# Optimization experiments

Measured on AMD Instinct MI355X. Metric: run time of the kernel, lower is better.

The kernel has to match this reference:

```python
import jax, jax.numpy as jnp
import numpy as np

N = 4096   # num_nodes == nb_items
E = 3      # num_edge types
C = 2      # num_channels
D = 128    # basket_embed_dim
RU = 128   # rnn_units
B = 32     # batch size
L = 20     # max_seq_length
ALPHA = 0.5


def _gtconv(W, A):
    # softmax over edge types, then channel-weighted combine of adjacencies
    f = jax.nn.softmax(W, axis=1)              # [C, E]
    return jnp.einsum('ce,enm->cnm', f, A)     # [C, N, N]


def _normalize(H):
    # remove self loops, then column-degree (in-degree) inverse normalization
    eye = jnp.eye(H.shape[-1], dtype=H.dtype)
    Hn = H * (1.0 - eye)
    deg = Hn.sum(axis=1)                        # scatter_add over col -> [C, N]
    dinv = jnp.where(deg == 0, jnp.zeros_like(deg), 1.0 / deg)
    dinv = jax.lax.stop_gradient(dinv)          # original computes deg under no_grad
    return Hn * dinv[:, None, :]


def _lstm(x, h0, c0, W_ih, W_hh, b_ih, b_hh):
    # single-layer batch-first LSTM, torch gate order (i, f, g, o)
    def step(carry, xt):
        h, c = carry
        z = xt @ W_ih.T + b_ih + h @ W_hh.T + b_hh
        i, f, g, o = jnp.split(z, 4, axis=-1)
        c = jax.nn.sigmoid(f) * c + jax.nn.sigmoid(i) * jnp.tanh(g)
        h = jax.nn.sigmoid(o) * jnp.tanh(c)
        return (h, c), h
    _, ys = jax.lax.scan(step, (h0, c0), jnp.swapaxes(x, 0, 1))
    return jnp.swapaxes(ys, 0, 1)               # [B, L, RU]


def setup_inputs():
    key = jax.random.key(0)
    k = jax.random.split(key, 12)
    A = jax.random.uniform(k[0], (E, N, N), jnp.float32) * (2.0 / N)
    seqs = (jax.random.uniform(k[1], (B, L, N)) < 0.02).astype(jnp.float32)
    seq_len = jax.random.randint(k[2], (B,), 1, L + 1)
    h0 = jnp.zeros((B, RU), jnp.float32)
    c0 = jnp.zeros((B, RU), jnp.float32)
    W1a = 1.0 + 0.1 * jax.random.normal(k[3], (C, E), jnp.float32)
    W1b = 1.0 + 0.1 * jax.random.normal(k[4], (C, E), jnp.float32)
    W2 = 1.0 + 0.1 * jax.random.normal(k[5], (C, E), jnp.float32)
    I_B = jnp.ones((N,), jnp.float32) / N
    lin_w = jax.random.normal(k[6], (C, D, N), jnp.float32) / np.sqrt(N).astype(np.float32)
    lin_b = jnp.zeros((C, D), jnp.float32)
    proj_w = jax.random.normal(k[7], (D, C * D), jnp.float32) / np.sqrt(C * D).astype(np.float32)
    proj_b = jnp.zeros((D,), jnp.float32)
    W_ih = jax.random.normal(k[8], (4 * RU, D), jnp.float32) / np.sqrt(D).astype(np.float32)
    W_hh = jax.random.normal(k[9], (4 * RU, RU), jnp.float32) / np.sqrt(RU).astype(np.float32)
    b_ih = jnp.zeros((4 * RU,), jnp.float32)
    b_hh = jnp.zeros((4 * RU,), jnp.float32)
    h2item_w = jax.random.normal(k[10], (N, RU), jnp.float32) / np.sqrt(RU).astype(np.float32)
    return dict(A=A, seqs=seqs, seq_len=seq_len, h0=h0, c0=c0, W1a=W1a, W1b=W1b,
                W2=W2, I_B=I_B, lin_w=lin_w, lin_b=lin_b, proj_w=proj_w, proj_b=proj_b,
                W_ih=W_ih, W_hh=W_hh, b_ih=b_ih, b_hh=b_hh, h2item_w=h2item_w)


def reference(A, seqs, seq_len, h0, c0, W1a, W1b, W2, I_B, lin_w, lin_b,
              proj_w, proj_b, W_ih, W_hh, b_ih, b_hh, h2item_w):
    # layer 0 (first=True): H[c] = conv1(A)[c] @ conv2(A)[c]  (spspmm, dense form)
    H = jnp.einsum('cij,cjk->cik', _gtconv(W1a, A), _gtconv(W1b, A))
    # layer 1: H[c] = norm(H)[c] @ conv(A)[c]
    H = jnp.einsum('cij,cjk->cik', _normalize(H), _gtconv(W2, A))

    x = seqs.reshape(-1, N)                     # [B*L, nb_items]
    v = jax.nn.relu(I_B)                        # diag(I_B) after relu
    enc = []
    for i in range(C):
        xh = jax.nn.relu(x @ H[i])
        if i == 0:
            e = jax.nn.relu(x * v) + xh         # note: channel-0 formula differs
        else:
            e = jax.nn.relu(x * v + xh)
        enc.append(e @ lin_w[i].T + lin_b[i])
    enc = jnp.concatenate(enc, axis=1)          # [B*L, C*D]
    baskets = (enc @ proj_w.T + proj_b).reshape(B, L, D)

    lstm_out = _lstm(baskets, h0, c0, W_ih, W_hh, b_ih, b_hh)
    idx = jnp.arange(B) * L + (seq_len - 1)
    last = lstm_out.reshape(-1, RU)[idx]        # [B, RU]
    probs = jax.nn.sigmoid(last @ h2item_w.T)   # [B, nb_items]
    return (1.0 - ALPHA) * probs + ALPHA * (probs * v)
```

## Files before the change

kernel.cpp:

```cpp
#include <hip/hip_runtime.h>


typedef float  f4v  __attribute__((ext_vector_type(4)));
typedef short  s8v  __attribute__((ext_vector_type(8)));
typedef unsigned short u16;
typedef u16    us4  __attribute__((ext_vector_type(4)));

#define NN 4096
#define MM 640

__device__ __forceinline__ u16 f2bf(float f){
  unsigned int u = __float_as_uint(f);
  u += 0x7FFFu + ((u>>16)&1u);
  return (u16)(u>>16);
}
__device__ __forceinline__ float bf2f(u16 h){ return __uint_as_float(((unsigned int)h)<<16); }
__device__ __forceinline__ float sigm(float x){ return 1.f/(1.f+__expf(-x)); }

__device__ __forceinline__ void gload16(const void* g, void* l){
  __builtin_amdgcn_global_load_lds((const __attribute__((address_space(1))) unsigned int*)g,
                                   (__attribute__((address_space(3))) unsigned int*)l, 16, 0, 0);
}

__device__ __forceinline__ void softmax23(const float* __restrict__ W, float f[2][3]){
  #pragma unroll
  for (int c=0;c<2;c++){
    float a=W[c*3+0], b=W[c*3+1], d=W[c*3+2];
    float m=fmaxf(a,fmaxf(b,d));
    float ea=__expf(a-m), eb=__expf(b-m), ed=__expf(d-m);
    float s=1.f/(ea+eb+ed);
    f[c][0]=ea*s; f[c][1]=eb*s; f[c][2]=ed*s;
  }
}

template<int PH3>
__global__ __launch_bounds__(256)
void k_combine(const float* __restrict__ A, const float* __restrict__ Wa,
               const float* __restrict__ Wb, u16* __restrict__ C1,
               u16* __restrict__ Ct, float* __restrict__ r)
{
  __shared__ u16 t2[2][64][68];
  __shared__ float rs[2][64];
  const int tid = threadIdx.x;
  const int n0 = blockIdx.x*64, m0 = blockIdx.y*64;
  float fa[2][3], fb[2][3];
  softmax23(Wa, fa);
  if constexpr(!PH3) softmax23(Wb, fb);
  if constexpr(!PH3){ if (tid < 128) rs[tid>>6][tid&63] = 0.f; }
  __syncthreads();
  const int cl = (tid&15)*4, rw0 = tid>>4;
  float rp[2][4] = {};
  #pragma unroll
  for (int q=0;q<4;q++){
    const int m = q*16 + rw0;
    const float* ap = A + (size_t)(m0+m)*NN + n0 + cl;
    f4v a0 = *(const f4v*)ap;
    f4v a1 = *(const f4v*)(ap + (size_t)NN*NN);
    f4v a2 = *(const f4v*)(ap + 2*(size_t)NN*NN);
    #pragma unroll
    for (int c=0;c<2;c++){
      f4v vt;
      if constexpr(!PH3){
        f4v v1 = fa[c][0]*a0 + fa[c][1]*a1 + fa[c][2]*a2;
        vt     = fb[c][0]*a0 + fb[c][1]*a1 + fb[c][2]*a2;
        us4 o;
        #pragma unroll
        for (int k=0;k<4;k++){ o[k]=f2bf(v1[k]); rp[c][k]+=v1[k]; }
        *(us4*)(C1 + ((size_t)c*NN + m0+m)*NN + n0+cl) = o;
      } else {
        vt = fa[c][0]*a0 + fa[c][1]*a1 + fa[c][2]*a2;
      }
      #pragma unroll
      for (int k=0;k<4;k++) t2[c][cl+k][m] = f2bf(vt[k]);
    }
  }
  if constexpr(!PH3){
    #pragma unroll
    for (int c=0;c<2;c++)
      #pragma unroll
      for (int k=0;k<4;k++) atomicAdd(&rs[c][cl+k], rp[c][k]);
  }
  __syncthreads();
  if constexpr(!PH3){
    if (tid < 128) atomicAdd(&r[(size_t)(tid>>6)*NN + n0 + (tid&63)], rs[tid>>6][tid&63]);
  }
  #pragma unroll
  for (int q=0;q<4;q++){
    const int nl = q*16 + rw0;
    #pragma unroll
    for (int c=0;c<2;c++){
      us4 o = *(const us4*)&t2[c][nl][cl];
      *(us4*)(Ct + ((size_t)c*NN + n0+nl)*NN + m0+cl) = o;
    }
  }
}

__global__ __launch_bounds__(256)
void k_sparse_y(const float* __restrict__ seqs, const u16* __restrict__ C1,
                u16* __restrict__ y)
{
  __shared__ int idxl[512];
  __shared__ int cnt;
  const int tid = threadIdx.x, row = blockIdx.x;
  if (tid==0) cnt = 0;
  __syncthreads();
  const float* xr = seqs + (size_t)row*NN;
  #pragma unroll
  for (int it=0; it<4; ++it){
    f4v v = *(const f4v*)(xr + it*1024 + tid*4);
    #pragma unroll
    for (int k=0;k<4;k++) if (v[k] > 0.5f){ int p = atomicAdd(&cnt,1); if (p<512) idxl[p] = it*1024+tid*4+k; }
  }
  __syncthreads();
  const int nz = cnt < 512 ? cnt : 512;
  float acc0[16], acc1[16];
  #pragma unroll
  for (int k=0;k<16;k++){ acc0[k]=0.f; acc1[k]=0.f; }
  const int cb = tid*16;
  for (int p=0;p<nz;++p){
    const u16* r0 = C1 + (size_t)idxl[p]*NN + cb;
    const u16* r1 = r0 + (size_t)NN*NN;
    s8v a = *(const s8v*)r0, b = *(const s8v*)(r0+8);
    s8v c = *(const s8v*)r1, d = *(const s8v*)(r1+8);
    #pragma unroll
    for (int k=0;k<8;k++){
      acc0[k]   += bf2f((u16)a[k]);
      acc0[8+k] += bf2f((u16)b[k]);
      acc1[k]   += bf2f((u16)c[k]);
      acc1[8+k] += bf2f((u16)d[k]);
    }
  }
  s8v o0,o1,o2,o3;
  #pragma unroll
  for (int k=0;k<8;k++){
    o0[k]=(short)f2bf(acc0[k]);   o1[k]=(short)f2bf(acc0[8+k]);
    o2[k]=(short)f2bf(acc1[k]);   o3[k]=(short)f2bf(acc1[8+k]);
  }
  u16* y0 = y + (size_t)row*NN + cb;
  *(s8v*)y0 = o0; *(s8v*)(y0+8) = o1;
  u16* y1 = y0 + (size_t)MM*NN;
  *(s8v*)y1 = o2; *(s8v*)(y1+8) = o3;
}

__global__ __launch_bounds__(256)
void k_diagdeg(const u16* __restrict__ C1, const u16* __restrict__ C2t,
               const float* __restrict__ r, float* __restrict__ diag1,
               float* __restrict__ dinv)
{
  const int tid = threadIdx.x, lane = tid&63;
  const int gw = blockIdx.x*4 + (tid>>6);
  const int c = gw>>12, k = gw&4095;
  const u16* p1 = C1  + ((size_t)c*NN + k)*NN;
  const u16* p2 = C2t + ((size_t)c*NN + k)*NN;
  const float* pr = r + (size_t)c*NN;
  float dd = 0.f, dg = 0.f;
  for (int it=0; it<8; ++it){
    const int j = it*512 + lane*8;
    s8v v1 = *(const s8v*)(p1+j);
    s8v v2 = *(const s8v*)(p2+j);
    f4v r0 = *(const f4v*)(pr+j);
    f4v r1 = *(const f4v*)(pr+j+4);
    #pragma unroll
    for (int q=0;q<8;q++){
      float c2 = bf2f((u16)v2[q]);
      dd += bf2f((u16)v1[q]) * c2;
      dg += ((q<4)? r0[q] : r1[q-4]) * c2;
    }
  }
  #pragma unroll
  for (int m=1;m<64;m<<=1){ dd += __shfl_xor(dd, m); dg += __shfl_xor(dg, m); }
  if (lane==0){
    float deg = dg - dd;
    diag1[(size_t)c*NN+k] = dd;
    dinv[(size_t)c*NN+k]  = (deg==0.f) ? 0.f : 1.f/deg;
  }
}

template<int EPI>
__global__ __launch_bounds__(256)
void k_gemm(const u16* __restrict__ Xb, const u16* __restrict__ Bt,
            const float* __restrict__ seqs, const float* __restrict__ diag1,
            const float* __restrict__ dinv, const float* __restrict__ IB,
            u16* __restrict__ outp)
{
  __shared__ u16 As[128*32];
  __shared__ u16 Bs[128*32];
  const int tid = threadIdx.x, lane = tid&63, w = tid>>6;
  const int c = blockIdx.z, m0 = blockIdx.x*128, n0 = blockIdx.y*128;
  const u16* Ab = Xb + (size_t)c*MM*NN;
  const u16* Bb = Bt + (size_t)c*NN*NN;
  const int srow = lane>>2, skof = (lane&3)*8;
  const int fr = lane&15, fk = (lane>>4)*8;
  const int wm = (w>>1)*64, wn = (w&1)*64;
  f4v acc[4][4];
  #pragma unroll
  for (int i=0;i<4;i++)
    #pragma unroll
    for (int j=0;j<4;j++) acc[i][j] = (f4v){0.f,0.f,0.f,0.f};
  for (int k0=0;k0<NN;k0+=32){
    gload16(Ab + (size_t)(m0 +      w*16 + srow)*NN + k0 + skof, (void*)&As[(     w*16)*32]);
    gload16(Ab + (size_t)(m0 + 64 + w*16 + srow)*NN + k0 + skof, (void*)&As[(64 + w*16)*32]);
    gload16(Bb + (size_t)(n0 +      w*16 + srow)*NN + k0 + skof, (void*)&Bs[(     w*16)*32]);
    gload16(Bb + (size_t)(n0 + 64 + w*16 + srow)*NN + k0 + skof, (void*)&Bs[(64 + w*16)*32]);
    __syncthreads();
    s8v a[4], b[4];
    #pragma unroll
    for (int t=0;t<4;t++) a[t] = *(const s8v*)&As[(wm + t*16 + fr)*32 + fk];
    #pragma unroll
    for (int t=0;t<4;t++) b[t] = *(const s8v*)&Bs[(wn + t*16 + fr)*32 + fk];
    #pragma unroll
    for (int i=0;i<4;i++)
      #pragma unroll
      for (int j=0;j<4;j++)
        acc[i][j] = __builtin_amdgcn_mfma_f32_16x16x32_bf16(a[i], b[j], acc[i][j], 0, 0, 0);
    __syncthreads();
  }
  #pragma unroll
  for (int i=0;i<4;i++){
    #pragma unroll
    for (int j=0;j<4;j++){
      const int col = n0 + wn + j*16 + fr;
      #pragma unroll
      for (int rr=0;rr<4;rr++){
        const int row = m0 + wm + i*16 + (lane>>4)*4 + rr;
        const float z = acc[i][j][rr];
        const float x = seqs[(size_t)row*NN + col];
        float val;
        if constexpr(EPI==0){
          val = (z - x*diag1[(size_t)c*NN+col]) * dinv[(size_t)c*NN+col];
        } else {
          float xh = fmaxf(z, 0.f);
          float vv = fmaxf(IB[col], 0.f);
          val = (c==0) ? (fmaxf(x*vv,0.f) + xh) : fmaxf(x*vv + xh, 0.f);
        }
        outp[((size_t)c*MM + row)*NN + col] = f2bf(val);
      }
    }
  }
}

__global__ __launch_bounds__(256)
void k_cvt(const float* __restrict__ linw, const float* __restrict__ whh,
           u16* __restrict__ linwb, u16* __restrict__ whhb)
{
  const int g = blockIdx.x*256 + threadIdx.x;
  const int i = g*4;
  const int NL = 2*128*NN;
  f4v v; u16* dst;
  if (i < NL){ v = *(const f4v*)(linw + i); dst = linwb + i; }
  else       { v = *(const f4v*)(whh + (i-NL)); dst = whhb + (i-NL); }
  us4 o;
  #pragma unroll
  for (int k=0;k<4;k++) o[k]=f2bf(v[k]);
  *(us4*)dst = o;
}

__global__ __launch_bounds__(256)
void k_lin(const u16* __restrict__ e, const u16* __restrict__ linwb,
           float* __restrict__ encr)
{
  __shared__ u16 As[64*32];
  __shared__ u16 Bs[64*32];
  const int tid=threadIdx.x, lane=tid&63, w=tid>>6;
  const int m0 = blockIdx.x*64, d0 = blockIdx.y*64;
  const int c = blockIdx.z>>2, ks = blockIdx.z&3;
  const u16* Ab = e + (size_t)c*MM*NN;
  const u16* Bb = linwb + (size_t)c*128*NN;
  const int srow=lane>>2, skof=(lane&3)*8, fr=lane&15, fk=(lane>>4)*8;
  const int wm=(w>>1)*32, wn=(w&1)*32;
  f4v acc[2][2];
  #pragma unroll
  for (int i=0;i<2;i++)
    #pragma unroll
    for (int j=0;j<2;j++) acc[i][j] = (f4v){0.f,0.f,0.f,0.f};
  for (int ki=0;ki<32;++ki){
    const int k0 = ks*1024 + ki*32;
    gload16(Ab + (size_t)(m0 + w*16 + srow)*NN + k0 + skof, (void*)&As[(w*16)*32]);
    gload16(Bb + (size_t)(d0 + w*16 + srow)*NN + k0 + skof, (void*)&Bs[(w*16)*32]);
    __syncthreads();
    s8v a[2], b[2];
    #pragma unroll
    for (int t=0;t<2;t++) a[t] = *(const s8v*)&As[(wm+t*16+fr)*32+fk];
    #pragma unroll
    for (int t=0;t<2;t++) b[t] = *(const s8v*)&Bs[(wn+t*16+fr)*32+fk];
    #pragma unroll
    for (int i=0;i<2;i++)
      #pragma unroll
      for (int j=0;j<2;j++)
        acc[i][j] = __builtin_amdgcn_mfma_f32_16x16x32_bf16(a[i], b[j], acc[i][j], 0, 0, 0);
    __syncthreads();
  }
  #pragma unroll
  for (int i=0;i<2;i++)
    #pragma unroll
    for (int j=0;j<2;j++){
      const int col = d0 + wn + j*16 + fr;
      #pragma unroll
      for (int rr=0;rr<4;rr++){
        const int row = m0 + wm + i*16 + (lane>>4)*4 + rr;
        atomicAdd(&encr[(size_t)row*256 + c*128 + col], acc[i][j][rr]);
      }
    }
}

__global__ __launch_bounds__(256)
void k_proj(const float* __restrict__ encr, const float* __restrict__ linb,
            const float* __restrict__ pw, const float* __restrict__ pb,
            float* __restrict__ bask)
{
  const int g = blockIdx.x*256 + threadIdx.x;
  const int row = g>>7, d = g&127;
  const float* er = encr + (size_t)row*256;
  const float* wr = pw + (size_t)d*256;
  float acc = pb[d];
  for (int j=0;j<256;j+=4){
    f4v e4 = *(const f4v*)(er+j);
    f4v l4 = *(const f4v*)(linb+j);
    f4v w4 = *(const f4v*)(wr+j);
    acc += (e4[0]+l4[0])*w4[0] + (e4[1]+l4[1])*w4[1] + (e4[2]+l4[2])*w4[2] + (e4[3]+l4[3])*w4[3];
  }
  bask[g] = acc;
}

__global__ __launch_bounds__(256)
void k_xhat(const float* __restrict__ bask, const float* __restrict__ wih,
            const float* __restrict__ bih, const float* __restrict__ bhh,
            float* __restrict__ xh)
{
  const int g = blockIdx.x*256 + threadIdx.x;
  const int row = g>>9, n = g&511;
  const float* br = bask + (size_t)row*128;
  const float* wr = wih + (size_t)n*128;
  float acc = bih[n] + bhh[n];
  for (int k=0;k<128;k+=4){
    f4v b4=*(const f4v*)(br+k); f4v w4=*(const f4v*)(wr+k);
    acc += b4[0]*w4[0]+b4[1]*w4[1]+b4[2]*w4[2]+b4[3]*w4[3];
  }
  const int b = row/20, t = row%20;
  xh[((size_t)t*32 + b)*512 + n] = acc;
}

__global__ __launch_bounds__(512)
void k_lstm(const float* __restrict__ xhat, const u16* __restrict__ whhb,
            const float* __restrict__ h0, const float* __restrict__ c0,
            const int* __restrict__ slen, float* __restrict__ last)
{
  __shared__ float zb[32][512];
  __shared__ float cbuf[32][128];
  __shared__ u16 hb[32][136];
  const int tid = threadIdx.x, lane = tid&63, w = tid>>6;
  for (int i=tid; i<4096; i+=512){ int b=i>>7,u=i&127; cbuf[b][u]=c0[i]; hb[b][u]=f2bf(h0[i]); }
  const int fr = lane&15, fko = (lane>>4)*8;
  s8v bfr[4][4];
  #pragma unroll
  for (int nt=0;nt<4;nt++)
    #pragma unroll
    for (int kf=0;kf<4;kf++)
      bfr[nt][kf] = *(const s8v*)(whhb + (size_t)(w*64 + nt*16 + fr)*128 + kf*32 + fko);
  __syncthreads();
  for (int t=0;t<20;++t){
    s8v af[2][4];
    #pragma unroll
    for (int mt=0;mt<2;mt++)
      #pragma unroll
      for (int kf=0;kf<4;kf++)
        af[mt][kf] = *(const s8v*)&hb[mt*16+fr][kf*32+fko];
    f4v z[2][4];
    #pragma unroll
    for (int mt=0;mt<2;mt++)
      #pragma unroll
      for (int nt=0;nt<4;nt++){
        const int nn2 = w*64 + nt*16 + fr;
        #pragma unroll
        for (int rr=0;rr<4;rr++){
          const int bb = mt*16 + (lane>>4)*4 + rr;
          z[mt][nt][rr] = xhat[((size_t)t*32 + bb)*512 + nn2];
        }
      }
    #pragma unroll
    for (int kf=0;kf<4;kf++)
      #pragma unroll
      for (int mt=0;mt<2;mt++)
        #pragma unroll
        for (int nt=0;nt<4;nt++)
          z[mt][nt] = __builtin_amdgcn_mfma_f32_16x16x32_bf16(af[mt][kf], bfr[nt][kf], z[mt][nt], 0, 0, 0);
    #pragma unroll
    for (int mt=0;mt<2;mt++)
      #pragma unroll
      for (int nt=0;nt<4;nt++){
        const int nn2 = w*64 + nt*16 + fr;
        #pragma unroll
        for (int rr=0;rr<4;rr++){
          const int bb = mt*16 + (lane>>4)*4 + rr;
          zb[bb][nn2] = z[mt][nt][rr];
        }
      }
    __syncthreads();
    for (int p=tid; p<4096; p+=512){
      const int b=p>>7, u=p&127;
      float zi=zb[b][u], zf=zb[b][128+u], zg=zb[b][256+u], zo=zb[b][384+u];
      float ii=sigm(zi), ff=sigm(zf), gg=tanhf(zg), oo=sigm(zo);
      float cn = ff*cbuf[b][u] + ii*gg;
      float hn = oo*tanhf(cn);
      cbuf[b][u]=cn; hb[b][u]=f2bf(hn);
      if (t == slen[b]-1) last[p] = hn;
    }
    __syncthreads();
  }
}

__global__ __launch_bounds__(256)
void k_final(const float* __restrict__ last, const float* __restrict__ h2w,
             const float* __restrict__ IB, float* __restrict__ out)
{
  __shared__ float ls[128];
  const int b = blockIdx.y;
  const int n = blockIdx.x*256 + threadIdx.x;
  if (threadIdx.x < 128) ls[threadIdx.x] = last[b*128 + threadIdx.x];
  __syncthreads();
  const float* wr = h2w + (size_t)n*128;
  float acc = 0.f;
  for (int k=0;k<128;k+=4){
    f4v w4 = *(const f4v*)(wr+k);
    acc += w4[0]*ls[k] + w4[1]*ls[k+1] + w4[2]*ls[k+2] + w4[3]*ls[k+3];
  }
  const float vn = fmaxf(IB[n], 0.f);
  out[(size_t)b*NN + n] = (0.5f + 0.5f*vn) * sigm(acc);
}

extern "C" void kernel_launch(void* const* d_in, const int* in_sizes, int n_in,
                              void* d_out, int out_size, void* d_ws, size_t ws_size,
                              hipStream_t stream)
{
  const float* A    = (const float*)d_in[0];
  const float* seqs = (const float*)d_in[1];
  const int*   slen = (const int*)  d_in[2];
  const float* h0   = (const float*)d_in[3];
  const float* c0   = (const float*)d_in[4];
  const float* W1a  = (const float*)d_in[5];
  const float* W1b  = (const float*)d_in[6];
  const float* W2   = (const float*)d_in[7];
  const float* IB   = (const float*)d_in[8];
  const float* linw = (const float*)d_in[9];
  const float* linb = (const float*)d_in[10];
  const float* pw   = (const float*)d_in[11];
  const float* pb   = (const float*)d_in[12];
  const float* wih  = (const float*)d_in[13];
  const float* whh  = (const float*)d_in[14];
  const float* bih  = (const float*)d_in[15];
  const float* bhh  = (const float*)d_in[16];
  const float* h2w  = (const float*)d_in[17];
  (void)in_sizes; (void)n_in; (void)out_size; (void)ws_size;

  char* ws = (char*)d_ws;
  size_t off = 0;
  auto alloc = [&](size_t sz)->void*{ void* p = ws + off; off += (sz + 255) & ~(size_t)255; return p; };
  u16*   C1    = (u16*)  alloc((size_t)2*NN*NN*2);
  u16*   C2t   = (u16*)  alloc((size_t)2*NN*NN*2);
  u16*   y     = (u16*)  alloc((size_t)2*MM*NN*2);
  u16*   u     = (u16*)  alloc((size_t)2*MM*NN*2);
  float* r     = (float*)alloc((size_t)2*NN*4);
  float* diag1 = (float*)alloc((size_t)2*NN*4);
  float* dinv  = (float*)alloc((size_t)2*NN*4);
  u16*   linwb = (u16*)  alloc((size_t)2*128*NN*2);
  u16*   whhb  = (u16*)  alloc((size_t)512*128*2);
  float* encr  = (float*)alloc((size_t)MM*256*4);
  float* bask  = (float*)alloc((size_t)MM*128*4);
  float* xh    = (float*)alloc((size_t)20*32*512*4);
  float* last  = (float*)alloc((size_t)32*128*4);

  hipMemsetAsync(r, 0, (size_t)2*NN*4, stream);
  hipMemsetAsync(encr, 0, (size_t)MM*256*4, stream);

  k_combine<0><<<dim3(64,64),256,0,stream>>>(A, W1a, W1b, C1, C2t, r);
  k_sparse_y<<<MM,256,0,stream>>>(seqs, C1, y);
  k_diagdeg<<<2048,256,0,stream>>>(C1, C2t, r, diag1, dinv);
  k_gemm<0><<<dim3(5,32,2),256,0,stream>>>(y, C2t, seqs, diag1, dinv, IB, u);
  k_combine<1><<<dim3(64,64),256,0,stream>>>(A, W2, W2, C1, C1, r);
  u16* e = y;
  k_gemm<1><<<dim3(5,32,2),256,0,stream>>>(u, C1, seqs, diag1, dinv, IB, e);
  k_cvt<<<1088,256,0,stream>>>(linw, whh, linwb, whhb);
  k_lin<<<dim3(10,2,8),256,0,stream>>>(e, linwb, encr);
  k_proj<<<320,256,0,stream>>>(encr, linb, pw, pb, bask);
  k_xhat<<<1280,256,0,stream>>>(bask, wih, bih, bhh, xh);
  k_lstm<<<1,512,0,stream>>>(xh, whhb, h0, c0, slen, last);
  k_final<<<dim3(16,32),256,0,stream>>>(last, h2w, IB, (float*)d_out);
}
```

Before: 629.8 us.

## Fuse all three adjacency combines into one pass and retile the bf16 GEMMs

Merges the two combine kernels so the 3×N×N fp32 adjacency is read once and emits C1, C2t and a new C3t buffer together. This removes a second full pass over the large A tensor at the cost of an extra workspace buffer. The main GEMM moves to 64x64 tiles with K=64 steps and an XOR-swizzled LDS layout, giving more blocks and fewer bank conflicts. The epilogue scalar loads are hoisted out of the inner loop. Smaller changes add packed bf16 conversion instructions, register prefetch in the sparse-row gather, and a 4x larger split-K for k_lin.

```diff
diff --git a/kernel.cpp b/kernel.cpp
--- a/kernel.cpp
+++ b/kernel.cpp
@@ -5,6 +5,9 @@
 typedef short  s8v  __attribute__((ext_vector_type(8)));
 typedef unsigned short u16;
 typedef u16    us4  __attribute__((ext_vector_type(4)));
+typedef unsigned int u32;
+typedef u32    u2v  __attribute__((ext_vector_type(2)));
+typedef u32    u4v  __attribute__((ext_vector_type(4)));
 
 #define NN 4096
 #define MM 640
@@ -16,6 +19,12 @@
 }
 __device__ __forceinline__ float bf2f(u16 h){ return __uint_as_float(((unsigned int)h)<<16); }
 __device__ __forceinline__ float sigm(float x){ return 1.f/(1.f+__expf(-x)); }
+
+__device__ __forceinline__ u32 pkbf(float lo, float hi){
+  u32 r;
+  asm("v_cvt_pk_bf16_f32 %0, %1, %2" : "=v"(r) : "v"(lo), "v"(hi));
+  return r;
+}
 
 __device__ __forceinline__ void gload16(const void* g, void* l){
   __builtin_amdgcn_global_load_lds((const __attribute__((address_space(1))) unsigned int*)g,
@@ -33,64 +42,79 @@
   }
 }
 
-template<int PH3>
-__global__ __launch_bounds__(256)
-void k_combine(const float* __restrict__ A, const float* __restrict__ Wa,
-               const float* __restrict__ Wb, u16* __restrict__ C1,
-               u16* __restrict__ Ct, float* __restrict__ r)
+__global__ __launch_bounds__(256)
+void k_combine_all(const float* __restrict__ A, const float* __restrict__ W1a,
+                   const float* __restrict__ W1b, const float* __restrict__ W2,
+                   u16* __restrict__ C1, u16* __restrict__ C2t,
+                   u16* __restrict__ C3t, float* __restrict__ r)
 {
   __shared__ u16 t2[2][64][68];
+  __shared__ u16 t3[2][64][68];
   __shared__ float rs[2][64];
-  const int tid = threadIdx.x;
+  const int tid = threadIdx.x, lane = tid&63;
   const int n0 = blockIdx.x*64, m0 = blockIdx.y*64;
-  float fa[2][3], fb[2][3];
-  softmax23(Wa, fa);
-  if constexpr(!PH3) softmax23(Wb, fb);
-  if constexpr(!PH3){ if (tid < 128) rs[tid>>6][tid&63] = 0.f; }
+  float fa[2][3], fb[2][3], fc[2][3];
+  softmax23(W1a, fa); softmax23(W1b, fb); softmax23(W2, fc);
+  if (tid < 128) rs[tid>>6][tid&63] = 0.f;
   __syncthreads();
-  const int cl = (tid&15)*4, rw0 = tid>>4;
+  const int mb = tid>>4, nb = tid&15;
+  f4v a0[4], a1[4], a2[4];
+  #pragma unroll
+  for (int j=0;j<4;j++){
+    const float* ap = A + (size_t)(m0+mb*4+j)*NN + n0 + nb*4;
+    a0[j] = *(const f4v*)ap;
+    a1[j] = *(const f4v*)(ap + (size_t)NN*NN);
+    a2[j] = *(const f4v*)(ap + 2*(size_t)NN*NN);
+  }
   float rp[2][4] = {};
   #pragma unroll
-  for (int q=0;q<4;q++){
-    const int m = q*16 + rw0;
-    const float* ap = A + (size_t)(m0+m)*NN + n0 + cl;
-    f4v a0 = *(const f4v*)ap;
-    f4v a1 = *(const f4v*)(ap + (size_t)NN*NN);
-    f4v a2 = *(const f4v*)(ap + 2*(size_t)NN*NN);
-    #pragma unroll
-    for (int c=0;c<2;c++){
-      f4v vt;
-      if constexpr(!PH3){
-        f4v v1 = fa[c][0]*a0 + fa[c][1]*a1 + fa[c][2]*a2;
-        vt     = fb[c][0]*a0 + fb[c][1]*a1 + fb[c][2]*a2;
-        us4 o;
-        #pragma unroll
-        for (int k=0;k<4;k++){ o[k]=f2bf(v1[k]); rp[c][k]+=v1[k]; }
-        *(us4*)(C1 + ((size_t)c*NN + m0+m)*NN + n0+cl) = o;
-      } else {
-        vt = fa[c][0]*a0 + fa[c][1]*a1 + fa[c][2]*a2;
-      }
-      #pragma unroll
-      for (int k=0;k<4;k++) t2[c][cl+k][m] = f2bf(vt[k]);
-    }
-  }
-  if constexpr(!PH3){
-    #pragma unroll
-    for (int c=0;c<2;c++)
-      #pragma unroll
-      for (int k=0;k<4;k++) atomicAdd(&rs[c][cl+k], rp[c][k]);
-  }
+  for (int c=0;c<2;c++){
+    f4v v1[4], vt[4], v3[4];
+    #pragma unroll
+    for (int j=0;j<4;j++){
+      v1[j] = fa[c][0]*a0[j] + fa[c][1]*a1[j] + fa[c][2]*a2[j];
+      vt[j] = fb[c][0]*a0[j] + fb[c][1]*a1[j] + fb[c][2]*a2[j];
+      v3[j] = fc[c][0]*a0[j] + fc[c][1]*a1[j] + fc[c][2]*a2[j];
+    }
+    #pragma unroll
+    for (int j=0;j<4;j++){
+      u2v o = { pkbf(v1[j][0],v1[j][1]), pkbf(v1[j][2],v1[j][3]) };
+      *(u2v*)(C1 + ((size_t)c*NN + m0+mb*4+j)*NN + n0 + nb*4) = o;
+      #pragma unroll
+      for (int k=0;k<4;k++) rp[c][k] += v1[j][k];
+    }
+    #pragma unroll
+    for (int jj=0;jj<4;jj++){
+      u2v o2 = { pkbf(vt[0][jj],vt[1][jj]), pkbf(vt[2][jj],vt[3][jj]) };
+      u2v o3 = { pkbf(v3[0][jj],v3[1][jj]), pkbf(v3[2][jj],v3[3][jj]) };
+      *(u2v*)&t2[c][nb*4+jj][mb*4] = o2;
+      *(u2v*)&t3[c][nb*4+jj][mb*4] = o3;
+    }
+  }
+  #pragma unroll
+  for (int c=0;c<2;c++)
+    #pragma unroll
+    for (int k=0;k<4;k++){
+      float v = rp[c][k];
+      v += __shfl_xor(v,16); v += __shfl_xor(v,32);
+      if (lane < 16) atomicAdd(&rs[c][(lane&15)*4+k], v);
+    }
   __syncthreads();
-  if constexpr(!PH3){
-    if (tid < 128) atomicAdd(&r[(size_t)(tid>>6)*NN + n0 + (tid&63)], rs[tid>>6][tid&63]);
-  }
-  #pragma unroll
-  for (int q=0;q<4;q++){
-    const int nl = q*16 + rw0;
-    #pragma unroll
-    for (int c=0;c<2;c++){
-      us4 o = *(const us4*)&t2[c][nl][cl];
-      *(us4*)(Ct + ((size_t)c*NN + n0+nl)*NN + m0+cl) = o;
+  if (tid < 128) atomicAdd(&r[(size_t)(tid>>6)*NN + n0 + (tid&63)], rs[tid>>6][tid&63]);
+  const int nl = tid>>2, mc = tid&3;
+  #pragma unroll
+  for (int c=0;c<2;c++){
+    #pragma unroll
+    for (int rep=0;rep<2;rep++){
+      const int cc = mc + rep*4;
+      u2v lo2 = *(const u2v*)&t2[c][nl][cc*8];
+      u2v hi2 = *(const u2v*)&t2[c][nl][cc*8+4];
+      u4v o2 = { lo2[0], lo2[1], hi2[0], hi2[1] };
+      *(u4v*)(C2t + ((size_t)c*NN + n0+nl)*NN + m0 + cc*8) = o2;
+      u2v lo3 = *(const u2v*)&t3[c][nl][cc*8];
+      u2v hi3 = *(const u2v*)&t3[c][nl][cc*8+4];
+      u4v o3 = { lo3[0], lo3[1], hi3[0], hi3[1] };
+      *(u4v*)(C3t + ((size_t)c*NN + n0+nl)*NN + m0 + cc*8) = o3;
     }
   }
 }
@@ -117,29 +141,41 @@
   #pragma unroll
   for (int k=0;k<16;k++){ acc0[k]=0.f; acc1[k]=0.f; }
   const int cb = tid*16;
+  s8v ca, cb8, cc8, cd8;
+  if (nz > 0){
+    const u16* r0 = C1 + (size_t)idxl[0]*NN + cb;
+    const u16* r1 = r0 + (size_t)NN*NN;
+    ca=*(const s8v*)r0; cb8=*(const s8v*)(r0+8); cc8=*(const s8v*)r1; cd8=*(const s8v*)(r1+8);
+  }
   for (int p=0;p<nz;++p){
-    const u16* r0 = C1 + (size_t)idxl[p]*NN + cb;
+    const int pn = (p+1<nz)? p+1 : p;
+    const u16* r0 = C1 + (size_t)idxl[pn]*NN + cb;
     const u16* r1 = r0 + (size_t)NN*NN;
-    s8v a = *(const s8v*)r0, b = *(const s8v*)(r0+8);
-    s8v c = *(const s8v*)r1, d = *(const s8v*)(r1+8);
+    s8v na=*(const s8v*)r0, nb=*(const s8v*)(r0+8), nc=*(const s8v*)r1, nd=*(const s8v*)(r1+8);
     #pragma unroll
     for (int k=0;k<8;k++){
-      acc0[k]   += bf2f((u16)a[k]);
-      acc0[8+k] += bf2f((u16)b[k]);
-      acc1[k]   += bf2f((u16)c[k]);
-      acc1[8+k] += bf2f((u16)d[k]);
-    }
-  }
-  s8v o0,o1,o2,o3;
-  #pragma unroll
-  for (int k=0;k<8;k++){
-    o0[k]=(short)f2bf(acc0[k]);   o1[k]=(short)f2bf(acc0[8+k]);
-    o2[k]=(short)f2bf(acc1[k]);   o3[k]=(short)f2bf(acc1[8+k]);
+      acc0[k]   += bf2f((u16)ca[k]);
+      acc0[8+k] += bf2f((u16)cb8[k]);
+      acc1[k]   += bf2f((u16)cc8[k]);
+      acc1[8+k] += bf2f((u16)cd8[k]);
+    }
+    ca=na; cb8=nb; cc8=nc; cd8=nd;
+  }
+  u4v o0, o1;
+  #pragma unroll
+  for (int k=0;k<4;k++){
+    o0[k] = pkbf(acc0[2*k], acc0[2*k+1]);
+    o1[k] = pkbf(acc0[8+2*k], acc0[9+2*k]);
   }
   u16* y0 = y + (size_t)row*NN + cb;
-  *(s8v*)y0 = o0; *(s8v*)(y0+8) = o1;
+  *(u4v*)y0 = o0; *(u4v*)(y0+8) = o1;
+  #pragma unroll
+  for (int k=0;k<4;k++){
+    o0[k] = pkbf(acc1[2*k], acc1[2*k+1]);
+    o1[k] = pkbf(acc1[8+2*k], acc1[9+2*k]);
+  }
   u16* y1 = y0 + (size_t)MM*NN;
-  *(s8v*)y1 = o2; *(s8v*)(y1+8) = o3;
+  *(u4v*)y1 = o0; *(u4v*)(y1+8) = o1;
 }
 
 __global__ __launch_bounds__(256)
@@ -178,48 +214,56 @@
 
 template<int EPI>
 __global__ __launch_bounds__(256)
-void k_gemm(const u16* __restrict__ Xb, const u16* __restrict__ Bt,
-            const float* __restrict__ seqs, const float* __restrict__ diag1,
-            const float* __restrict__ dinv, const float* __restrict__ IB,
-            u16* __restrict__ outp)
-{
-  __shared__ u16 As[128*32];
-  __shared__ u16 Bs[128*32];
+void k_gemmf(const u16* __restrict__ Xb, const u16* __restrict__ Bt,
+             const float* __restrict__ seqs, const float* __restrict__ diag1,
+             const float* __restrict__ dinv, const float* __restrict__ IB,
+             u16* __restrict__ outp)
+{
+  __shared__ u16 As[64*64];
+  __shared__ u16 Bs[64*64];
   const int tid = threadIdx.x, lane = tid&63, w = tid>>6;
-  const int c = blockIdx.z, m0 = blockIdx.x*128, n0 = blockIdx.y*128;
+  const int m0 = blockIdx.x*64, n0 = blockIdx.y*64;
+  const int c = blockIdx.z;
   const u16* Ab = Xb + (size_t)c*MM*NN;
   const u16* Bb = Bt + (size_t)c*NN*NN;
-  const int srow = lane>>2, skof = (lane&3)*8;
-  const int fr = lane&15, fk = (lane>>4)*8;
-  const int wm = (w>>1)*64, wn = (w&1)*64;
-  f4v acc[4][4];
-  #pragma unroll
-  for (int i=0;i<4;i++)
-    #pragma unroll
-    for (int j=0;j<4;j++) acc[i][j] = (f4v){0.f,0.f,0.f,0.f};
-  for (int k0=0;k0<NN;k0+=32){
-    gload16(Ab + (size_t)(m0 +      w*16 + srow)*NN + k0 + skof, (void*)&As[(     w*16)*32]);
-    gload16(Ab + (size_t)(m0 + 64 + w*16 + srow)*NN + k0 + skof, (void*)&As[(64 + w*16)*32]);
-    gload16(Bb + (size_t)(n0 +      w*16 + srow)*NN + k0 + skof, (void*)&Bs[(     w*16)*32]);
-    gload16(Bb + (size_t)(n0 + 64 + w*16 + srow)*NN + k0 + skof, (void*)&Bs[(64 + w*16)*32]);
+  const int srow = lane>>3;
+  const int scol = ((lane&7) ^ (srow&7))*8;
+  const int fr = lane&15, fkq = lane>>4;
+  const int wm = (w>>1)*32, wn = (w&1)*32;
+  f4v acc[2][2] = {};
+  for (int k0=0;k0<NN;k0+=64){
+    #pragma unroll
+    for (int t=0;t<2;t++){
+      gload16(Ab + (size_t)(m0 + t*32 + w*8 + srow)*NN + k0 + scol, (void*)&As[(t*32 + w*8)*64]);
+      gload16(Bb + (size_t)(n0 + t*32 + w*8 + srow)*NN + k0 + scol, (void*)&Bs[(t*32 + w*8)*64]);
+    }
     __syncthreads();
-    s8v a[4], b[4];
-    #pragma unroll
-    for (int t=0;t<4;t++) a[t] = *(const s8v*)&As[(wm + t*16 + fr)*32 + fk];
-    #pragma unroll
-    for (int t=0;t<4;t++) b[t] = *(const s8v*)&Bs[(wn + t*16 + fr)*32 + fk];
-    #pragma unroll
-    for (int i=0;i<4;i++)
-      #pragma unroll
-      for (int j=0;j<4;j++)
-        acc[i][j] = __builtin_amdgcn_mfma_f32_16x16x32_bf16(a[i], b[j], acc[i][j], 0, 0, 0);
+    #pragma unroll
+    for (int kk=0;kk<2;kk++){
+      s8v a[2], b[2];
+      #pragma unroll
+      for (int t=0;t<2;t++){
+        const int ra = wm + t*16 + fr;
+        a[t] = *(const s8v*)&As[ra*64 + (((kk*4 + fkq) ^ (ra&7))*8)];
+        const int rb = wn + t*16 + fr;
+        b[t] = *(const s8v*)&Bs[rb*64 + (((kk*4 + fkq) ^ (rb&7))*8)];
+      }
+      #pragma unroll
+      for (int i=0;i<2;i++)
+        #pragma unroll
+        for (int j=0;j<2;j++)
+          acc[i][j] = __builtin_amdgcn_mfma_f32_16x16x32_bf16(a[i], b[j], acc[i][j], 0, 0, 0);
+    }
     __syncthreads();
   }
   #pragma unroll
-  for (int i=0;i<4;i++){
-    #pragma unroll
-    for (int j=0;j<4;j++){
+  for (int i=0;i<2;i++){
+    #pragma unroll
+    for (int j=0;j<2;j++){
       const int col = n0 + wn + j*16 + fr;
+      float dg, dv, vv;
+      if constexpr(EPI==0){ dg = diag1[(size_t)c*NN+col]; dv = dinv[(size_t)c*NN+col]; }
+      else                { vv = fmaxf(IB[col], 0.f); }
       #pragma unroll
       for (int rr=0;rr<4;rr++){
         const int row = m0 + wm + i*16 + (lane>>4)*4 + rr;
@@ -227,10 +271,9 @@
         const float x = seqs[(size_t)row*NN + col];
         float val;
         if constexpr(EPI==0){
-          val = (z - x*diag1[(size_t)c*NN+col]) * dinv[(size_t)c*NN+col];
+          val = (z - x*dg) * dv;
         } else {
           float xh = fmaxf(z, 0.f);
-          float vv = fmaxf(IB[col], 0.f);
           val = (c==0) ? (fmaxf(x*vv,0.f) + xh) : fmaxf(x*vv + xh, 0.f);
         }
         outp[((size_t)c*MM + row)*NN + col] = f2bf(val);
@@ -249,10 +292,8 @@
   f4v v; u16* dst;
   if (i < NL){ v = *(const f4v*)(linw + i); dst = linwb + i; }
   else       { v = *(const f4v*)(whh + (i-NL)); dst = whhb + (i-NL); }
-  us4 o;
-  #pragma unroll
-  for (int k=0;k<4;k++) o[k]=f2bf(v[k]);
-  *(us4*)dst = o;
+  u2v o = { pkbf(v[0],v[1]), pkbf(v[2],v[3]) };
+  *(u2v*)dst = o;
 }
 
 __global__ __launch_bounds__(256)
@@ -263,7 +304,7 @@
   __shared__ u16 Bs[64*32];
   const int tid=threadIdx.x, lane=tid&63, w=tid>>6;
   const int m0 = blockIdx.x*64, d0 = blockIdx.y*64;
-  const int c = blockIdx.z>>2, ks = blockIdx.z&3;
+  const int c = blockIdx.z>>4, ks = blockIdx.z&15;
   const u16* Ab = e + (size_t)c*MM*NN;
   const u16* Bb = linwb + (size_t)c*128*NN;
   const int srow=lane>>2, skof=(lane&3)*8, fr=lane&15, fk=(lane>>4)*8;
@@ -273,8 +314,8 @@
   for (int i=0;i<2;i++)
     #pragma unroll
     for (int j=0;j<2;j++) acc[i][j] = (f4v){0.f,0.f,0.f,0.f};
-  for (int ki=0;ki<32;++ki){
-    const int k0 = ks*1024 + ki*32;
+  for (int ki=0;ki<8;++ki){
+    const int k0 = ks*256 + ki*32;
     gload16(Ab + (size_t)(m0 + w*16 + srow)*NN + k0 + skof, (void*)&As[(w*16)*32]);
     gload16(Bb + (size_t)(d0 + w*16 + srow)*NN + k0 + skof, (void*)&Bs[(w*16)*32]);
     __syncthreads();
@@ -457,6 +498,7 @@
   auto alloc = [&](size_t sz)->void*{ void* p = ws + off; off += (sz + 255) & ~(size_t)255; return p; };
   u16*   C1    = (u16*)  alloc((size_t)2*NN*NN*2);
   u16*   C2t   = (u16*)  alloc((size_t)2*NN*NN*2);
+  u16*   C3t   = (u16*)  alloc((size_t)2*NN*NN*2);
   u16*   y     = (u16*)  alloc((size_t)2*MM*NN*2);
   u16*   u     = (u16*)  alloc((size_t)2*MM*NN*2);
   float* r     = (float*)alloc((size_t)2*NN*4);
@@ -472,15 +514,14 @@
   hipMemsetAsync(r, 0, (size_t)2*NN*4, stream);
   hipMemsetAsync(encr, 0, (size_t)MM*256*4, stream);
 
-  k_combine<0><<<dim3(64,64),256,0,stream>>>(A, W1a, W1b, C1, C2t, r);
+  k_combine_all<<<dim3(64,64),256,0,stream>>>(A, W1a, W1b, W2, C1, C2t, C3t, r);
   k_sparse_y<<<MM,256,0,stream>>>(seqs, C1, y);
   k_diagdeg<<<2048,256,0,stream>>>(C1, C2t, r, diag1, dinv);
-  k_gemm<0><<<dim3(5,32,2),256,0,stream>>>(y, C2t, seqs, diag1, dinv, IB, u);
-  k_combine<1><<<dim3(64,64),256,0,stream>>>(A, W2, W2, C1, C1, r);
+  k_gemmf<0><<<dim3(10,64,2),256,0,stream>>>(y, C2t, seqs, diag1, dinv, IB, u);
   u16* e = y;
-  k_gemm<1><<<dim3(5,32,2),256,0,stream>>>(u, C1, seqs, diag1, dinv, IB, e);
+  k_gemmf<1><<<dim3(10,64,2),256,0,stream>>>(u, C3t, seqs, diag1, dinv, IB, e);
   k_cvt<<<1088,256,0,stream>>>(linw, whh, linwb, whhb);
-  k_lin<<<dim3(10,2,8),256,0,stream>>>(e, linwb, encr);
+  k_lin<<<dim3(10,2,32),256,0,stream>>>(e, linwb, encr);
   k_proj<<<320,256,0,stream>>>(encr, linb, pw, pb, bask);
   k_xhat<<<1280,256,0,stream>>>(bask, wih, bih, bhh, xh);
   k_lstm<<<1,512,0,stream>>>(xh, whhb, h0, c0, slen, last);
```

Result: faster. 549.4 us (-12.8%).
